# Kernel tuning notes

Measured on AMD Instinct MI355X. Metric: run time of the kernel, lower is better.

The kernel has to match this reference:

```python
import jax, jax.numpy as jnp
import numpy as np

N = 100000      # nodes (accounts)
E = 500000      # edges (transactions)
F_NODE = 128
F_EDGE = 32
HEADS = 4
C = 64          # hidden_channels per head
HC = HEADS * C  # 256
OUT = 32
BN_EPS = 1e-5
NEG_SLOPE = 0.2


def setup_inputs() -> dict:
    key = jax.random.key(0)
    ks = jax.random.split(key, 24)
    rn = lambda k, shape, s=0.05: (jax.random.normal(k, shape, jnp.float32) * s)
    inp = {
        "x": jax.random.normal(ks[0], (N, F_NODE), jnp.float32),
        "edge_index": jax.random.randint(ks[1], (2, E), 0, N, dtype=jnp.int32),
        "edge_attr": jax.random.normal(ks[2], (E, F_EDGE), jnp.float32),
        # node_proj
        "Wp": rn(ks[3], (F_NODE, C)), "bp": jnp.zeros((C,), jnp.float32),
    }
    in_dims = [C, HC, HC]
    i = 4
    for l, d in enumerate(in_dims):
        inp[f"Wg{l}"] = rn(ks[i], (d, HC)); i += 1
        inp[f"as{l}"] = rn(ks[i], (HEADS, C)); i += 1
        inp[f"ad{l}"] = rn(ks[i], (HEADS, C)); i += 1
        inp[f"bg{l}"] = jnp.zeros((HC,), jnp.float32)
        inp[f"g{l}"] = jnp.ones((HC,), jnp.float32)   # BN gamma
        inp[f"be{l}"] = jnp.zeros((HC,), jnp.float32)  # BN beta
    inp["W1"] = rn(ks[i], (2 * HC + F_EDGE, OUT)); inp["b1"] = jnp.zeros((OUT,), jnp.float32)
    inp["W2"] = rn(ks[i + 1], (OUT, 1)); inp["b2"] = jnp.zeros((1,), jnp.float32)
    return inp


def _gat_layer(h, src, dst, Wg, att_s, att_d, bg):
    # PyG GATConv (concat=True, add_self_loops=False), eval mode (no dropout).
    xh = (h @ Wg).reshape(N, HEADS, C)                      # [N,H,C]
    a_s = jnp.sum(xh * att_s, axis=-1)                      # [N,H]
    a_d = jnp.sum(xh * att_d, axis=-1)                      # [N,H]
    e = jax.nn.leaky_relu(a_s[src] + a_d[dst], NEG_SLOPE)   # [E,H]
    m = jax.lax.stop_gradient(jax.ops.segment_max(e, dst, num_segments=N))
    ex = jnp.exp(e - m[dst])
    den = jax.ops.segment_sum(ex, dst, num_segments=N)      # [N,H]
    alpha = ex / (den[dst] + 1e-16)                         # softmax over in-edges of dst
    agg = jax.ops.segment_sum(xh[src] * alpha[:, :, None], dst, num_segments=N)
    return agg.reshape(N, HC) + bg


def _forward(x, edge_index, edge_attr, Wp, bp,
             Wg0, as0, ad0, bg0, g0, be0,
             Wg1, as1, ad1, bg1, g1, be1,
             Wg2, as2, ad2, bg2, g2, be2,
             W1, b1, W2, b2):
    src, dst = edge_index[0], edge_index[1]
    h = jax.nn.relu(x @ Wp + bp)                            # [N,64]
    bn_scale = 1.0 / jnp.sqrt(jnp.float32(1.0) + BN_EPS)    # BN eval: mean=0, var=1
    layers = [(Wg0, as0, ad0, bg0, g0, be0),
              (Wg1, as1, ad1, bg1, g1, be1),
              (Wg2, as2, ad2, bg2, g2, be2)]
    for Wg, a_s, a_d, bg, g, be in layers:
        hn = _gat_layer(h, src, dst, Wg, a_s, a_d, bg)
        hn = jax.nn.relu(hn * (g * bn_scale) + be)          # BatchNorm(eval) + ReLU
        h = h + hn if h.shape == hn.shape else hn           # residual (skipped at layer 0)
    # decode_edges: MLP(src_emb || dst_emb || edge_attr) without materializing the concat:
    W1s, W1d, W1e = W1[:HC], W1[HC:2 * HC], W1[2 * HC:]
    z = jax.nn.relu((h @ W1s)[src] + (h @ W1d)[dst] + edge_attr @ W1e + b1)  # [E,32]
    return (z @ W2 + b2)[:, 0]                              # [E] fraud logits


def reference(x, edge_index, edge_attr, Wp, bp,
              Wg0, as0, ad0, bg0, g0, be0,
              Wg1, as1, ad1, bg1, g1, be1,
              Wg2, as2, ad2, bg2, g2, be2,
              W1, b1, W2, b2):
    return _forward(x, edge_index, edge_attr, Wp, bp,
                    Wg0, as0, ad0, bg0, g0, be0,
                    Wg1, as1, ad1, bg1, g1, be1,
                    Wg2, as2, ad2, bg2, g2, be2,
                    W1, b1, W2, b2)
```

## Files before the change

### kernel.cpp

```cpp
#include <hip/hip_runtime.h>
#include <hip/hip_fp16.h>

#define NN 100000
#define EE 500000
#define F_NODE 128
#define F_EDGE 32
#define HEADS 4
#define CC 64
#define HC 256
#define OUTD 32
#define NEG_SLOPE 0.2f
#define BN_SCALE 0.9999950000374997f
#define NB_SCAN 391
#define MPAD 100096

using half8 = __attribute__((ext_vector_type(8))) _Float16;
using f32x4 = __attribute__((ext_vector_type(4))) float;

typedef const __attribute__((address_space(1))) void* gas_ptr;
typedef __attribute__((address_space(3))) void* las_ptr;

template<int K, int NOUT, int MODE>
__global__ __launch_bounds__(256, 2) void mgemm2(const __half* __restrict__ A,
                                                 const __half* __restrict__ Wt,
                                                 const float* __restrict__ bias,
                                                 __half* __restrict__ C) {
    constexpr int BM = 128;
    constexpr int BN = (NOUT >= 128) ? 128 : 64;
    constexpr int MI = 4;
    constexpr int NI = BN / 32;
    constexpr int KS = K / 64;
    constexpr int ABYTES = BM * 128;
    constexpr int BBYTES = BN * 128;
    __shared__ char smem[2 * (ABYTES + BBYTES)];

    const int tid  = threadIdx.x;
    const int wave = tid >> 6, lane = tid & 63;
    const int wr = wave >> 1, wc = wave & 1;
    const int lrow = lane & 15, kq = lane >> 4;
    const int m0 = blockIdx.x * BM;
    const int n0 = blockIdx.y * BN;
    const int srow = tid >> 3;
    const int sunit = tid & 7;
    const int wofs = (tid & 192) * 16;

    auto stage = [&](int buf, int ks) {
        char* base = smem + buf * (ABYTES + BBYTES);
        const int kk = ks * 64;
#pragma unroll
        for (int it = 0; it < BM / 32; ++it) {
            const int r = srow + it * 32;
            const __half* src = A + (size_t)(m0 + r) * K + kk + ((sunit ^ (r & 7)) << 3);
            __builtin_amdgcn_global_load_lds((gas_ptr)src,
                (las_ptr)(base + it * 4096 + wofs), 16, 0, 0);
        }
#pragma unroll
        for (int it = 0; it < BN / 32; ++it) {
            const int r = srow + it * 32;
            const __half* src = Wt + (size_t)(n0 + r) * K + kk + ((sunit ^ (r & 7)) << 3);
            __builtin_amdgcn_global_load_lds((gas_ptr)src,
                (las_ptr)(base + ABYTES + it * 4096 + wofs), 16, 0, 0);
        }
    };

    f32x4 acc[MI][NI] = {};

    auto compute = [&](int buf) {
        const char* Ab = smem + buf * (ABYTES + BBYTES);
        const char* Bb = Ab + ABYTES;
#pragma unroll
        for (int k32 = 0; k32 < 2; ++k32) {
            const int ku = k32 * 4 + kq;
            half8 af[MI], bf[NI];
#pragma unroll
            for (int mi = 0; mi < MI; ++mi) {
                const int rr = wr * 64 + mi * 16 + lrow;
                af[mi] = *(const half8*)(Ab + rr * 128 + ((ku ^ (rr & 7)) << 4));
            }
#pragma unroll
            for (int ni = 0; ni < NI; ++ni) {
                const int rc = wc * (BN / 2) + ni * 16 + lrow;
                bf[ni] = *(const half8*)(Bb + rc * 128 + ((ku ^ (rc & 7)) << 4));
            }
#pragma unroll
            for (int mi = 0; mi < MI; ++mi)
#pragma unroll
                for (int ni = 0; ni < NI; ++ni)
                    acc[mi][ni] = __builtin_amdgcn_mfma_f32_16x16x32_f16(
                        af[mi], bf[ni], acc[mi][ni], 0, 0, 0);
        }
    };

    stage(0, 0);
    __syncthreads();
    int cur = 0;
#pragma unroll
    for (int ks = 0; ks < KS; ++ks) {
        if (ks + 1 < KS) stage(cur ^ 1, ks + 1);
        compute(cur);
        __syncthreads();
        cur ^= 1;
    }

    const int crow = kq * 4;
#pragma unroll
    for (int mi = 0; mi < MI; ++mi) {
#pragma unroll
        for (int ni = 0; ni < NI; ++ni) {
            const int col = n0 + wc * (BN / 2) + ni * 16 + lrow;
            float bcol = (MODE == 1) ? bias[col] : 0.f;
#pragma unroll
            for (int r = 0; r < 4; ++r) {
                float v = acc[mi][ni][r];
                if constexpr (MODE == 1) v = fmaxf(v + bcol, 0.f);
                const int row = m0 + wr * 64 + mi * 16 + crow + r;
                C[(size_t)row * NOUT + col] = __float2half(v);
            }
        }
    }
}

__global__ __launch_bounds__(256) void wt_conv(const float* __restrict__ W,
                                               __half* __restrict__ Wt,
                                               int K, int N) {
    int idx = blockIdx.x * 256 + threadIdx.x;
    if (idx >= K * N) return;
    int n = idx / K, k = idx % K;
    Wt[idx] = __float2half(W[k * N + n]);
}

__global__ __launch_bounds__(256) void wt_final(const float* __restrict__ W1,
                                                __half* __restrict__ Wt) {
    int idx = blockIdx.x * 256 + threadIdx.x;
    if (idx >= 64 * 256) return;
    int n = idx >> 8, k = idx & 255;
    float v = (n < 32) ? W1[k * 32 + n] : W1[(256 + k) * 32 + (n - 32)];
    Wt[idx] = __float2half(v);
}

__global__ __launch_bounds__(256) void cvt_x(const float* __restrict__ x,
                                             __half* __restrict__ x16) {
    int i = blockIdx.x * 256 + threadIdx.x;
    float4 v = ((const float4*)x)[i];
    __half2* o = (__half2*)x16 + (size_t)i * 2;
    o[0] = __floats2half2_rn(v.x, v.y);
    o[1] = __floats2half2_rn(v.z, v.w);
}

__global__ __launch_bounds__(256) void csr_count(const int* __restrict__ dst,
                                                 int* __restrict__ deg,
                                                 int* __restrict__ pos) {
    int e = blockIdx.x * 256 + threadIdx.x;
    if (e >= EE) return;
    pos[e] = atomicAdd(deg + dst[e], 1);
}

__device__ __forceinline__ int wave_incl_scan(int v, int lane) {
#pragma unroll
    for (int off = 1; off < 64; off <<= 1) {
        int t = __shfl_up(v, off, 64);
        if (lane >= off) v += t;
    }
    return v;
}

__global__ __launch_bounds__(256) void scan1(const int* __restrict__ deg,
                                             int* __restrict__ rowptr,
                                             int* __restrict__ bsum) {
    int tid = threadIdx.x, n = blockIdx.x * 256 + tid;
    int lane = tid & 63, wave = tid >> 6;
    int d = (n < NN) ? deg[n] : 0;
    int v = wave_incl_scan(d, lane);
    __shared__ int ws[4];
    if (lane == 63) ws[wave] = v;
    __syncthreads();
    int woff = 0;
    for (int w = 0; w < wave; ++w) woff += ws[w];
    int incl = v + woff;
    if (n < NN) rowptr[n] = incl - d;
    if (tid == 255) bsum[blockIdx.x] = incl;
}

__global__ __launch_bounds__(512) void scan2(const int* __restrict__ bsum,
                                             int* __restrict__ boff) {
    int t = threadIdx.x;
    int lane = t & 63, wave = t >> 6;
    int d = (t < NB_SCAN) ? bsum[t] : 0;
    int v = wave_incl_scan(d, lane);
    __shared__ int ws[8];
    if (lane == 63) ws[wave] = v;
    __syncthreads();
    int woff = 0;
    for (int w = 0; w < wave; ++w) woff += ws[w];
    if (t < NB_SCAN) boff[t] = v + woff - d;
}

__global__ __launch_bounds__(256) void scan3(int* __restrict__ rowptr,
                                             const int* __restrict__ boff) {
    int n = blockIdx.x * 256 + threadIdx.x;
    if (n == 0) rowptr[NN] = EE;
    if (n < NN) rowptr[n] += boff[blockIdx.x];
}

__global__ __launch_bounds__(256) void csr_scatter(const int* __restrict__ src,
                                                   const int* __restrict__ dst,
                                                   const int* __restrict__ rowptr,
                                                   const int* __restrict__ pos,
                                                   int* __restrict__ srcs) {
    int e = blockIdx.x * 256 + threadIdx.x;
    if (e >= EE) return;
    srcs[rowptr[dst[e]] + pos[e]] = src[e];
}

__global__ __launch_bounds__(256) void att_score(const __half* __restrict__ xh,
                                                 const float* __restrict__ as_,
                                                 const float* __restrict__ ad_,
                                                 float* __restrict__ a_s,
                                                 float* __restrict__ a_d) {
    const int lane = threadIdx.x & 63, wave = threadIdx.x >> 6;
    const int n = blockIdx.x * 4 + wave;
    const int c0 = lane * 4;

    float ws0 = as_[c0], ws1 = as_[c0 + 1], ws2 = as_[c0 + 2], ws3 = as_[c0 + 3];
    float wd0 = ad_[c0], wd1 = ad_[c0 + 1], wd2 = ad_[c0 + 2], wd3 = ad_[c0 + 3];

    const __half2* p = (const __half2*)(xh + (size_t)n * HC);
    __half2 v0 = p[lane * 2], v1 = p[lane * 2 + 1];
    float x0 = __low2float(v0), x1 = __high2float(v0);
    float x2 = __low2float(v1), x3 = __high2float(v1);

    float ss = x0 * ws0 + x1 * ws1 + x2 * ws2 + x3 * ws3;
    float dd = x0 * wd0 + x1 * wd1 + x2 * wd2 + x3 * wd3;
#pragma unroll
    for (int m = 8; m >= 1; m >>= 1) {
        ss += __shfl_xor(ss, m, 64);
        dd += __shfl_xor(dd, m, 64);
    }
    if ((lane & 15) == 0) {
        a_s[n * HEADS + (lane >> 4)] = ss;
        a_d[n * HEADS + (lane >> 4)] = dd;
    }
}

__global__ __launch_bounds__(256) void gather_agg(const int* __restrict__ rowptr,
                                                  const int* __restrict__ srcs,
                                                  const float* __restrict__ a_s,
                                                  const float* __restrict__ a_d,
                                                  const __half* __restrict__ xh,
                                                  const float* __restrict__ bg,
                                                  const float* __restrict__ g,
                                                  const float* __restrict__ be,
                                                  __half* __restrict__ h,
                                                  int residual) {
    const int n = blockIdx.x * 4 + (threadIdx.x >> 6);
    const int lane = threadIdx.x & 63;
    if (n >= NN) return;
    const int hl = lane >> 5;
    const int l5 = lane & 31;
    const int hd = l5 >> 3;
    const int c0 = l5 * 8;

    const int start = rowptr[n], end = rowptr[n + 1];
    const float adv = a_d[n * HEADS + hd];

    float acc[8] = {};
    float den = 0.f;

    for (int i = start + hl; i < end; i += 8) {
        int  j0 = i,                 j1 = (i + 2 < end) ? i + 2 : i;
        int  j2 = (i + 4 < end) ? i + 4 : i;
        int  j3 = (i + 6 < end) ? i + 6 : i;
        const int s0 = srcs[j0], s1 = srcs[j1], s2 = srcs[j2], s3 = srcs[j3];

        float v0 = a_s[s0 * HEADS + hd] + adv;
        float v1 = a_s[s1 * HEADS + hd] + adv;
        float v2 = a_s[s2 * HEADS + hd] + adv;
        float v3 = a_s[s3 * HEADS + hd] + adv;
        v0 = (v0 > 0.f) ? v0 : v0 * NEG_SLOPE;
        v1 = (v1 > 0.f) ? v1 : v1 * NEG_SLOPE;
        v2 = (v2 > 0.f) ? v2 : v2 * NEG_SLOPE;
        v3 = (v3 > 0.f) ? v3 : v3 * NEG_SLOPE;
        float e0 = __expf(v0);
        float e1 = (i + 2 < end) ? __expf(v1) : 0.f;
        float e2 = (i + 4 < end) ? __expf(v2) : 0.f;
        float e3 = (i + 6 < end) ? __expf(v3) : 0.f;

        half8 r0 = *(const half8*)(xh + (size_t)s0 * HC + c0);
        half8 r1 = *(const half8*)(xh + (size_t)s1 * HC + c0);
        half8 r2 = *(const half8*)(xh + (size_t)s2 * HC + c0);
        half8 r3 = *(const half8*)(xh + (size_t)s3 * HC + c0);

#pragma unroll
        for (int k = 0; k < 8; ++k)
            acc[k] += e0 * (float)r0[k] + e1 * (float)r1[k]
                    + e2 * (float)r2[k] + e3 * (float)r3[k];
        den += e0 + e1 + e2 + e3;
    }

    den += __shfl_xor(den, 32, 64);
#pragma unroll
    for (int k = 0; k < 8; ++k) acc[k] += __shfl_xor(acc[k], 32, 64);

    if (hl != 0) return;
    const float inv = 1.f / (den + 1e-16f);

    float bgv[8], gv[8], bev[8];
    *(float4*)(bgv)     = *(const float4*)(bg + c0);
    *(float4*)(bgv + 4) = *(const float4*)(bg + c0 + 4);
    *(float4*)(gv)      = *(const float4*)(g + c0);
    *(float4*)(gv + 4)  = *(const float4*)(g + c0 + 4);
    *(float4*)(bev)     = *(const float4*)(be + c0);
    *(float4*)(bev + 4) = *(const float4*)(be + c0 + 4);

    half8* hp = (half8*)(h + (size_t)n * HC + c0);
    float r[8];
#pragma unroll
    for (int k = 0; k < 8; ++k)
        r[k] = fmaxf((acc[k] * inv + bgv[k]) * (gv[k] * BN_SCALE) + bev[k], 0.f);
    if (residual) {
        half8 old = *hp;
#pragma unroll
        for (int k = 0; k < 8; ++k) r[k] += (float)old[k];
    }
    half8 o;
#pragma unroll
    for (int k = 0; k < 8; ++k) o[k] = (_Float16)r[k];
    *hp = o;
}

__global__ __launch_bounds__(256) void edge_final(const float* __restrict__ ea,
                                                  const __half* __restrict__ w1et,
                                                  const float* __restrict__ b1,
                                                  const int* __restrict__ src,
                                                  const int* __restrict__ dst,
                                                  const __half* __restrict__ hshd,
                                                  const float* __restrict__ W2,
                                                  const float* __restrict__ b2,
                                                  float* __restrict__ out) {
    __shared__ float zl[64][36];
    const int wave = threadIdx.x >> 6, lane = threadIdx.x & 63;
    const int e0 = blockIdx.x * 64;
    const int lrow = lane & 15, kofs = (lane >> 4) * 8;

    int er = e0 + wave * 16 + lrow;
    if (er >= EE) er = EE - 1;
    const float* ap = ea + (size_t)er * F_EDGE + kofs;
    float4 f0 = *(const float4*)ap;
    float4 f1 = *(const float4*)(ap + 4);
    half8 a;
    a[0] = (_Float16)f0.x; a[1] = (_Float16)f0.y;
    a[2] = (_Float16)f0.z; a[3] = (_Float16)f0.w;
    a[4] = (_Float16)f1.x; a[5] = (_Float16)f1.y;
    a[6] = (_Float16)f1.z; a[7] = (_Float16)f1.w;

    half8 b0 = *(const half8*)(w1et + (size_t)lrow * 32 + kofs);
    half8 b1v = *(const half8*)(w1et + (size_t)(16 + lrow) * 32 + kofs);
    f32x4 acc0 = {}, acc1 = {};
    acc0 = __builtin_amdgcn_mfma_f32_16x16x32_f16(a, b0,  acc0, 0, 0, 0);
    acc1 = __builtin_amdgcn_mfma_f32_16x16x32_f16(a, b1v, acc1, 0, 0, 0);

    const int crow = (lane >> 4) * 4;
    const float bc0 = b1[lrow], bc1 = b1[16 + lrow];
#pragma unroll
    for (int r = 0; r < 4; ++r) {
        zl[wave * 16 + crow + r][lrow]      = acc0[r] + bc0;
        zl[wave * 16 + crow + r][16 + lrow] = acc1[r] + bc1;
    }
    __syncthreads();

    const int el = threadIdx.x >> 2, j0 = (threadIdx.x & 3) * 8;
    const int e = e0 + el;
    const bool ok = e < EE;
    const int s = ok ? src[e] : 0;
    const int d = ok ? dst[e] : 0;

    half8 hs = *(const half8*)(hshd + (size_t)s * 64 + j0);
    half8 hdv = *(const half8*)(hshd + (size_t)d * 64 + 32 + j0);
    float w2v[8];
    *(float4*)(w2v)     = *(const float4*)(W2 + j0);
    *(float4*)(w2v + 4) = *(const float4*)(W2 + j0 + 4);
    float4 z0 = *(const float4*)&zl[el][j0];
    float4 z1 = *(const float4*)&zl[el][j0 + 4];

    float acc = 0.f;
    const float* zp0 = &z0.x;
    const float* zp1 = &z1.x;
#pragma unroll
    for (int i = 0; i < 4; ++i) {
        float z = zp0[i] + (float)hs[i] + (float)hdv[i];
        acc += fmaxf(z, 0.f) * w2v[i];
    }
#pragma unroll
    for (int i = 0; i < 4; ++i) {
        float z = zp1[i] + (float)hs[4 + i] + (float)hdv[4 + i];
        acc += fmaxf(z, 0.f) * w2v[4 + i];
    }
    acc += __shfl_xor(acc, 1, 64);
    acc += __shfl_xor(acc, 2, 64);
    if (ok && (threadIdx.x & 3) == 0) out[e] = acc + b2[0];
}

extern "C" void kernel_launch(void* const* d_in, const int* in_sizes, int n_in,
                              void* d_out, int out_size, void* d_ws, size_t ws_size,
                              hipStream_t stream) {
    const float* x  = (const float*)d_in[0];
    const int*   ei = (const int*)d_in[1];
    const float* ea = (const float*)d_in[2];
    const float* Wp = (const float*)d_in[3];
    const float* bp = (const float*)d_in[4];
    const float* W1 = (const float*)d_in[23];
    const float* b1 = (const float*)d_in[24];
    const float* W2 = (const float*)d_in[25];
    const float* b2 = (const float*)d_in[26];
    const int* src = ei;
    const int* dst = ei + EE;

    float* ws = (float*)d_ws;
    __half* h      = (__half*)(ws);
    __half* xh     = (__half*)(ws + 12820000);
    __half* x16    = (__half*)(ws + 25640000);
    __half* h0     = (__half*)(ws + 32050000);
    __half* hshd   = (__half*)(ws + 35260000);
    float*  a_s    = ws + 38470000;
    float*  a_d    = ws + 38870000;
    int*    rowptr = (int*)(ws + 41270000);
    int*    deg    = (int*)(ws + 41380000);
    int*    pos    = (int*)(ws + 41480000);
    int*    srcs   = (int*)(ws + 42490000);
    int*    bsum   = (int*)(ws + 42990000);
    int*    boff   = (int*)(ws + 42991000);
    __half* wpt    = (__half*)(ws + 42992000);
    __half* wgt    = (__half*)(ws + 43000000);
    __half* w1t    = (__half*)(ws + 43020000);
    float*  out    = (float*)d_out;

    const int MB = MPAD / 128;

    hipMemsetAsync(deg, 0, (size_t)NN * sizeof(int), stream);
    csr_count<<<(EE + 255) / 256, 256, 0, stream>>>(dst, deg, pos);
    scan1<<<NB_SCAN, 256, 0, stream>>>(deg, rowptr, bsum);
    scan2<<<1, 512, 0, stream>>>(bsum, boff);
    scan3<<<NB_SCAN, 256, 0, stream>>>(rowptr, boff);
    csr_scatter<<<(EE + 255) / 256, 256, 0, stream>>>(src, dst, rowptr, pos, srcs);

    cvt_x<<<NN * F_NODE / 4 / 256, 256, 0, stream>>>(x, x16);
    wt_conv<<<(F_NODE * 64 + 255) / 256, 256, 0, stream>>>(Wp, wpt, F_NODE, 64);

    mgemm2<F_NODE, 64, 1><<<dim3(MB, 1), 256, 0, stream>>>(x16, wpt, bp, h0);

    for (int l = 0; l < 3; ++l) {
        const float* Wg  = (const float*)d_in[5 + 6 * l];
        const float* as_ = (const float*)d_in[6 + 6 * l];
        const float* ad_ = (const float*)d_in[7 + 6 * l];
        const float* bg  = (const float*)d_in[8 + 6 * l];
        const float* g   = (const float*)d_in[9 + 6 * l];
        const float* be  = (const float*)d_in[10 + 6 * l];

        if (l == 0) {
            wt_conv<<<(CC * HC + 255) / 256, 256, 0, stream>>>(Wg, wgt, CC, HC);
            mgemm2<CC, HC, 0><<<dim3(MB, 2), 256, 0, stream>>>(h0, wgt, nullptr, xh);
        } else {
            wt_conv<<<(HC * HC + 255) / 256, 256, 0, stream>>>(Wg, wgt, HC, HC);
            mgemm2<HC, HC, 0><<<dim3(MB, 2), 256, 0, stream>>>(h, wgt, nullptr, xh);
        }

        att_score<<<NN / 4, 256, 0, stream>>>(xh, as_, ad_, a_s, a_d);
        gather_agg<<<(NN + 3) / 4, 256, 0, stream>>>(rowptr, srcs, a_s, a_d, xh,
                                                     bg, g, be, h, l > 0 ? 1 : 0);
    }

    wt_final<<<(64 * 256 + 255) / 256, 256, 0, stream>>>(W1, w1t);
    mgemm2<HC, 64, 0><<<dim3(MB, 1), 256, 0, stream>>>(h, w1t, nullptr, hshd);

    wt_conv<<<(32 * 32 + 255) / 256, 256, 0, stream>>>(W1 + 2 * HC * OUTD, wpt, 32, 32);
    edge_final<<<(EE + 63) / 64, 256, 0, stream>>>(ea, wpt, b1, src, dst, hshd, W2, b2, out);
}
```

Before: 409.4 us.

## Fuse attention score computation into GAT GEMM epilogue

Computes the per-head source and destination attention scores directly from the fp32 GEMM accumulators in the epilogue, using lane shuffles, and removes the separate att_score kernel. This saves one launch per layer and a full re-read of xh. The change also rewrites leaky-relu as an fmaxf and makes the final h write a nontemporal store. The a_d buffer is moved so the padded GEMM rows cannot overlap it. A side effect is that scores now come from fp32 accumulators rather than the fp16-rounded xh.

```diff
diff --git a/kernel.cpp b/kernel.cpp
--- a/kernel.cpp
+++ b/kernel.cpp
@@ -20,11 +20,15 @@
 typedef const __attribute__((address_space(1))) void* gas_ptr;
 typedef __attribute__((address_space(3))) void* las_ptr;
 
-template<int K, int NOUT, int MODE>
+template<int K, int NOUT, int MODE, int ATT>
 __global__ __launch_bounds__(256, 2) void mgemm2(const __half* __restrict__ A,
                                                  const __half* __restrict__ Wt,
                                                  const float* __restrict__ bias,
-                                                 __half* __restrict__ C) {
+                                                 __half* __restrict__ C,
+                                                 const float* __restrict__ as_,
+                                                 const float* __restrict__ ad_,
+                                                 float* __restrict__ a_s,
+                                                 float* __restrict__ a_d) {
     constexpr int BM = 128;
     constexpr int BN = (NOUT >= 128) ? 128 : 64;
     constexpr int MI = 4;
@@ -115,6 +119,39 @@
                 if constexpr (MODE == 1) v = fmaxf(v + bcol, 0.f);
                 const int row = m0 + wr * 64 + mi * 16 + crow + r;
                 C[(size_t)row * NOUT + col] = __float2half(v);
+            }
+        }
+    }
+
+    if constexpr (ATT) {
+        const int head = (n0 + wc * 64) >> 6;
+        float wsv[NI], wdv[NI];
+#pragma unroll
+        for (int ni = 0; ni < NI; ++ni) {
+            const int col = n0 + wc * (BN / 2) + ni * 16 + lrow;
+            wsv[ni] = as_[col];
+            wdv[ni] = ad_[col];
+        }
+#pragma unroll
+        for (int mi = 0; mi < MI; ++mi) {
+#pragma unroll
+            for (int r = 0; r < 4; ++r) {
+                float ss = 0.f, dd = 0.f;
+#pragma unroll
+                for (int ni = 0; ni < NI; ++ni) {
+                    ss += acc[mi][ni][r] * wsv[ni];
+                    dd += acc[mi][ni][r] * wdv[ni];
+                }
+#pragma unroll
+                for (int off = 8; off >= 1; off >>= 1) {
+                    ss += __shfl_xor(ss, off, 64);
+                    dd += __shfl_xor(dd, off, 64);
+                }
+                if (lrow == 0) {
+                    const int row = m0 + wr * 64 + mi * 16 + crow + r;
+                    a_s[row * HEADS + head] = ss;
+                    a_d[row * HEADS + head] = dd;
+                }
             }
         }
     }
@@ -210,36 +247,6 @@
     int e = blockIdx.x * 256 + threadIdx.x;
     if (e >= EE) return;
     srcs[rowptr[dst[e]] + pos[e]] = src[e];
-}
-
-__global__ __launch_bounds__(256) void att_score(const __half* __restrict__ xh,
-                                                 const float* __restrict__ as_,
-                                                 const float* __restrict__ ad_,
-                                                 float* __restrict__ a_s,
-                                                 float* __restrict__ a_d) {
-    const int lane = threadIdx.x & 63, wave = threadIdx.x >> 6;
-    const int n = blockIdx.x * 4 + wave;
-    const int c0 = lane * 4;
-
-    float ws0 = as_[c0], ws1 = as_[c0 + 1], ws2 = as_[c0 + 2], ws3 = as_[c0 + 3];
-    float wd0 = ad_[c0], wd1 = ad_[c0 + 1], wd2 = ad_[c0 + 2], wd3 = ad_[c0 + 3];
-
-    const __half2* p = (const __half2*)(xh + (size_t)n * HC);
-    __half2 v0 = p[lane * 2], v1 = p[lane * 2 + 1];
-    float x0 = __low2float(v0), x1 = __high2float(v0);
-    float x2 = __low2float(v1), x3 = __high2float(v1);
-
-    float ss = x0 * ws0 + x1 * ws1 + x2 * ws2 + x3 * ws3;
-    float dd = x0 * wd0 + x1 * wd1 + x2 * wd2 + x3 * wd3;
-#pragma unroll
-    for (int m = 8; m >= 1; m >>= 1) {
-        ss += __shfl_xor(ss, m, 64);
-        dd += __shfl_xor(dd, m, 64);
-    }
-    if ((lane & 15) == 0) {
-        a_s[n * HEADS + (lane >> 4)] = ss;
-        a_d[n * HEADS + (lane >> 4)] = dd;
-    }
 }
 
 __global__ __launch_bounds__(256) void gather_agg(const int* __restrict__ rowptr,
@@ -276,10 +283,10 @@
         float v1 = a_s[s1 * HEADS + hd] + adv;
         float v2 = a_s[s2 * HEADS + hd] + adv;
         float v3 = a_s[s3 * HEADS + hd] + adv;
-        v0 = (v0 > 0.f) ? v0 : v0 * NEG_SLOPE;
-        v1 = (v1 > 0.f) ? v1 : v1 * NEG_SLOPE;
-        v2 = (v2 > 0.f) ? v2 : v2 * NEG_SLOPE;
-        v3 = (v3 > 0.f) ? v3 : v3 * NEG_SLOPE;
+        v0 = fmaxf(v0, v0 * NEG_SLOPE);
+        v1 = fmaxf(v1, v1 * NEG_SLOPE);
+        v2 = fmaxf(v2, v2 * NEG_SLOPE);
+        v3 = fmaxf(v3, v3 * NEG_SLOPE);
         float e0 = __expf(v0);
         float e1 = (i + 2 < end) ? __expf(v1) : 0.f;
         float e2 = (i + 4 < end) ? __expf(v2) : 0.f;
@@ -325,7 +332,7 @@
     half8 o;
 #pragma unroll
     for (int k = 0; k < 8; ++k) o[k] = (_Float16)r[k];
-    *hp = o;
+    __builtin_nontemporal_store(o, hp);
 }
 
 __global__ __launch_bounds__(256) void edge_final(const float* __restrict__ ea,
@@ -422,7 +429,7 @@
     __half* h0     = (__half*)(ws + 32050000);
     __half* hshd   = (__half*)(ws + 35260000);
     float*  a_s    = ws + 38470000;
-    float*  a_d    = ws + 38870000;
+    float*  a_d    = ws + 38880000;
     int*    rowptr = (int*)(ws + 41270000);
     int*    deg    = (int*)(ws + 41380000);
     int*    pos    = (int*)(ws + 41480000);
@@ -446,7 +453,8 @@
     cvt_x<<<NN * F_NODE / 4 / 256, 256, 0, stream>>>(x, x16);
     wt_conv<<<(F_NODE * 64 + 255) / 256, 256, 0, stream>>>(Wp, wpt, F_NODE, 64);
 
-    mgemm2<F_NODE, 64, 1><<<dim3(MB, 1), 256, 0, stream>>>(x16, wpt, bp, h0);
+    mgemm2<F_NODE, 64, 1, 0><<<dim3(MB, 1), 256, 0, stream>>>(
+        x16, wpt, bp, h0, nullptr, nullptr, nullptr, nullptr);
 
     for (int l = 0; l < 3; ++l) {
         const float* Wg  = (const float*)d_in[5 + 6 * l];
@@ -458,19 +466,21 @@
 
         if (l == 0) {
             wt_conv<<<(CC * HC + 255) / 256, 256, 0, stream>>>(Wg, wgt, CC, HC);
-            mgemm2<CC, HC, 0><<<dim3(MB, 2), 256, 0, stream>>>(h0, wgt, nullptr, xh);
+            mgemm2<CC, HC, 0, 1><<<dim3(MB, 2), 256, 0, stream>>>(
+                h0, wgt, nullptr, xh, as_, ad_, a_s, a_d);
         } else {
             wt_conv<<<(HC * HC + 255) / 256, 256, 0, stream>>>(Wg, wgt, HC, HC);
-            mgemm2<HC, HC, 0><<<dim3(MB, 2), 256, 0, stream>>>(h, wgt, nullptr, xh);
-        }
-
-        att_score<<<NN / 4, 256, 0, stream>>>(xh, as_, ad_, a_s, a_d);
+            mgemm2<HC, HC, 0, 1><<<dim3(MB, 2), 256, 0, stream>>>(
+                h, wgt, nullptr, xh, as_, ad_, a_s, a_d);
+        }
+
         gather_agg<<<(NN + 3) / 4, 256, 0, stream>>>(rowptr, srcs, a_s, a_d, xh,
                                                      bg, g, be, h, l > 0 ? 1 : 0);
     }
 
     wt_final<<<(64 * 256 + 255) / 256, 256, 0, stream>>>(W1, w1t);
-    mgemm2<HC, 64, 0><<<dim3(MB, 1), 256, 0, stream>>>(h, w1t, nullptr, hshd);
+    mgemm2<HC, 64, 0, 0><<<dim3(MB, 1), 256, 0, stream>>>(
+        h, w1t, nullptr, hshd, nullptr, nullptr, nullptr, nullptr);
 
     wt_conv<<<(32 * 32 + 255) / 256, 256, 0, stream>>>(W1 + 2 * HC * OUTD, wpt, 32, 32);
     edge_final<<<(EE + 63) / 64, 256, 0, stream>>>(ea, wpt, b1, src, dst, hshd, W2, b2, out);
```

Result: faster. 393.8 us (-3.8%).
